# Performance work log

Hardware: AMD Instinct MI355X
Metric: run time of the kernel (lower is better)

## Reference

```python
import jax, jax.numpy as jnp
import numpy as np

N, E = 50000, 800000
F_IN, F_OUT, H, F_EDGE = 256, 32, 8, 5
LEAKY_SLOPE = 0.2


def setup_inputs() -> dict:
    key = jax.random.key(0)
    ks = jax.random.split(key, 6)
    x = jax.random.normal(ks[0], (N, F_IN), dtype=jnp.float32)
    edge_index = jax.random.randint(ks[1], (2, E), 0, N, dtype=jnp.int64)
    edge_attr = jax.random.normal(ks[2], (E, F_EDGE), dtype=jnp.float32)
    degree_src = jax.random.randint(ks[3], (E,), 0, 64, dtype=jnp.int64)
    # Xavier-uniform params
    lim_W = float(np.sqrt(6.0 / (F_IN + F_OUT)))
    W = jax.random.uniform(ks[4], (H, F_IN, F_OUT), minval=-lim_W, maxval=lim_W, dtype=jnp.float32)
    A = 2 * F_OUT + F_EDGE
    lim_a = float(np.sqrt(6.0 / (H + A)))
    a = jax.random.uniform(ks[5], (H, A), minval=-lim_a, maxval=lim_a, dtype=jnp.float32)
    lim_e = float(np.sqrt(1.0 / F_EDGE))
    W_edge_w = jax.random.uniform(jax.random.fold_in(key, 7), (F_EDGE, F_EDGE), minval=-lim_e, maxval=lim_e, dtype=jnp.float32)
    return {"x": x, "edge_index": edge_index, "edge_attr": edge_attr,
            "degree_src": degree_src, "W": W, "a": a, "W_edge_w": W_edge_w}


def reference(x, edge_index, edge_attr, degree_src, W, a, W_edge_w):
    n = x.shape[0]
    h, f_out = W.shape[0], W.shape[2]
    src, dst = edge_index[0], edge_index[1]
    # per-head projection: (N, H, F_out)
    Wh = jnp.einsum('nf,hfo->nho', x, W)
    # split attention vector instead of materializing the concat
    a_src, a_dst, a_e = a[:, :f_out], a[:, f_out:2 * f_out], a[:, 2 * f_out:]
    ef = edge_attr @ W_edge_w.T                      # (E, F_edge)
    e = (jnp.einsum('eho,ho->eh', Wh[src], a_src)
         + jnp.einsum('eho,ho->eh', Wh[dst], a_dst)
         + ef @ a_e.T)                                # (E, H)
    e = jax.nn.leaky_relu(e, LEAKY_SLOPE)
    scale = 1.0 / jnp.sqrt(jnp.clip(degree_src.astype(jnp.float32), 1.0, None))
    e = e * scale[:, None]
    # segment softmax over src; torch scatter_reduce amax include_self=True with zeros init -> max includes 0
    e_max = jnp.maximum(jax.ops.segment_max(e, src, num_segments=n), 0.0)
    e_exp = jnp.exp(e - e_max[src])
    e_sum = jax.ops.segment_sum(e_exp, src, num_segments=n)
    alpha = e_exp / (e_sum[src] + 1e-16)             # (E, H)
    msg = Wh[dst] * alpha[:, :, None]                # (E, H, F_out)
    out = jax.ops.segment_sum(msg, src, num_segments=n)
    out = jax.nn.elu(out.reshape(n, h * f_out))
    return out, alpha
```

## Files before the change

kernel.cpp:

```cpp
#include <hip/hip_runtime.h>
#include <hip/hip_bf16.h>
#include <math.h>

#define NN 50000
#define NE 800000
#define FIN 256
#define FOUT 32
#define NH 8
#define FE 5
#define AROW 69
#define NROWS_PAD 50048
#define NTILES 3128
#define BSTRIDE 48
#define CSTRIDE 264

typedef float f32x4 __attribute__((ext_vector_type(4)));
typedef short bf16x8 __attribute__((ext_vector_type(8)));

static __device__ __forceinline__ unsigned short f2bf(float f) {
    unsigned u = __float_as_uint(f);
    unsigned r = (u + 0x7FFFu + ((u >> 16) & 1u)) >> 16;
    return (unsigned short)r;
}
static __device__ __forceinline__ float bf2f(unsigned short b) {
    return __uint_as_float(((unsigned)b) << 16);
}
static __device__ __forceinline__ short f2bf_fast(float f) {
    __hip_bfloat16 h = __float2bfloat16(f);
    return *reinterpret_cast<short*>(&h);
}

__global__ __launch_bounds__(256) void k_prepre(const float* __restrict__ W,
                                                const float* __restrict__ a,
                                                const float* __restrict__ Wew,
                                                const float* __restrict__ x,
                                                const int* __restrict__ ei,
                                                float* __restrict__ C,
                                                unsigned short* __restrict__ Bhf,
                                                unsigned short* __restrict__ Bsfh,
                                                unsigned short* __restrict__ Bsfl,
                                                unsigned short* __restrict__ xbf,
                                                int* __restrict__ counts,
                                                int* __restrict__ pos) {
    int b = blockIdx.x, t = threadIdx.x;
    int j = b * 256 + t;
    if (j < NROWS_PAD * 32) {
        int row = j >> 5, seg = j & 31;
        bf16x8 hi;
#pragma unroll
        for (int e = 0; e < 8; ++e) hi[e] = 0;
        if (row < NN) {
            const float* sp = &x[(size_t)row * 256 + seg * 8];
            f32x4 u0 = *(const f32x4*)sp;
            f32x4 u1 = *(const f32x4*)(sp + 4);
            hi[0] = f2bf_fast(u0.x); hi[1] = f2bf_fast(u0.y);
            hi[2] = f2bf_fast(u0.z); hi[3] = f2bf_fast(u0.w);
            hi[4] = f2bf_fast(u1.x); hi[5] = f2bf_fast(u1.y);
            hi[6] = f2bf_fast(u1.z); hi[7] = f2bf_fast(u1.w);
        }
        int tile = row >> 4, r = row & 15;
        int ks = seg >> 2, blk = seg & 3;
        *(bf16x8*)&xbf[(size_t)tile * 4096 + ks * 512 + (blk * 16 + r) * 8] = hi;
    }
    if (j < NE / 4) {
        int4 e4 = *(const int4*)&ei[j * 4];
        int4 pv;
        pv.x = atomicAdd(&counts[e4.x], 1);
        pv.y = atomicAdd(&counts[e4.y], 1);
        pv.z = atomicAdd(&counts[e4.z], 1);
        pv.w = atomicAdd(&counts[e4.w], 1);
        *(int4*)&pos[j * 4] = pv;
    }
    if (b < 256) {
        int c = b, k = t;
        int h = c >> 5, o = c & 31;
        unsigned short val = f2bf(W[(size_t)h * (FIN * FOUT) + (size_t)k * FOUT + o]);
        int c_tile = c >> 4, rr = c & 15;
        int ks = k >> 5, bb = (k >> 3) & 3, e = k & 7;
        Bhf[(size_t)c_tile * 4096 + ks * 512 + (bb * 16 + rr) * 8 + e] = val;
    } else if (b == 256) {
        if (t < NH * FE) {
            int h = t / FE, k = t % FE;
            float s = 0.f;
            for (int q = 0; q < FE; ++q) s += a[h * AROW + 2 * FOUT + q] * Wew[q * FE + k];
            C[t] = s;
        }
        int k = t;
        int ks = k >> 5, bb = (k >> 3) & 3, e = k & 7;
        for (int h = 0; h < NH; ++h) {
            float s1v = 0.f, s2v = 0.f;
            for (int o = 0; o < FOUT; ++o) {
                float wv = W[(size_t)h * (FIN * FOUT) + (size_t)k * FOUT + o];
                s1v += wv * a[h * AROW + o];
                s2v += wv * a[h * AROW + FOUT + o];
            }
            unsigned short h1 = f2bf(s1v);
            unsigned short l1 = f2bf(s1v - bf2f(h1));
            unsigned short h2 = f2bf(s2v);
            unsigned short l2v = f2bf(s2v - bf2f(h2));
            Bsfh[ks * 512 + (bb * 16 + h) * 8 + e] = h1;
            Bsfl[ks * 512 + (bb * 16 + h) * 8 + e] = l1;
            Bsfh[ks * 512 + (bb * 16 + 8 + h) * 8 + e] = h2;
            Bsfl[ks * 512 + (bb * 16 + 8 + h) * 8 + e] = l2v;
        }
    }
}

__global__ __launch_bounds__(256) void k_gemm_mfma(const unsigned short* __restrict__ xbf,
                                                   const unsigned short* __restrict__ Bhf,
                                                   const unsigned short* __restrict__ Bsfh,
                                                   const unsigned short* __restrict__ Bsfl,
                                                   unsigned short* __restrict__ Whb,
                                                   float* __restrict__ s1,
                                                   float* __restrict__ s2, int nrows) {
    __shared__ __align__(16) unsigned short Ct[64 * CSTRIDE];
    int t = threadIdx.x;
    int w = t >> 6, l = t & 63;
    int r = l & 15, blk = l >> 4;
    int row0 = blockIdx.x * 64;
    int tile0 = blockIdx.x * 4;
    int c0 = w * 64;

    f32x4 acc[4][4];
    f32x4 acc_s = (f32x4)(0.f);
#pragma unroll
    for (int i = 0; i < 4; ++i)
#pragma unroll
        for (int q = 0; q < 4; ++q) acc[i][q] = (f32x4)(0.f);

    const unsigned short* pa[4];
    const unsigned short* pb[4];
#pragma unroll
    for (int rt = 0; rt < 4; ++rt)
        pa[rt] = xbf + (size_t)(tile0 + rt) * 4096 + l * 8;
#pragma unroll
    for (int ct = 0; ct < 4; ++ct)
        pb[ct] = Bhf + (size_t)(w * 4 + ct) * 4096 + l * 8;
    const unsigned short* psh = Bsfh + l * 8;
    const unsigned short* psl = Bsfl + l * 8;

#pragma unroll
    for (int ks = 0; ks < 8; ++ks) {
        bf16x8 ah[4];
#pragma unroll
        for (int rt = 0; rt < 4; ++rt)
            ah[rt] = *(const bf16x8*)(pa[rt] + ks * 512);
        bf16x8 bh[4];
#pragma unroll
        for (int ct = 0; ct < 4; ++ct)
            bh[ct] = *(const bf16x8*)(pb[ct] + ks * 512);
#pragma unroll
        for (int ct = 0; ct < 4; ++ct) {
#pragma unroll
            for (int rt = 0; rt < 4; ++rt)
                acc[rt][ct] = __builtin_amdgcn_mfma_f32_16x16x32_bf16(ah[rt], bh[ct], acc[rt][ct], 0, 0, 0);
        }
        {
            bf16x8 bsh = *(const bf16x8*)(psh + ks * 512);
            bf16x8 bsl = *(const bf16x8*)(psl + ks * 512);
            acc_s = __builtin_amdgcn_mfma_f32_16x16x32_bf16(ah[w], bsh, acc_s, 0, 0, 0);
            acc_s = __builtin_amdgcn_mfma_f32_16x16x32_bf16(ah[w], bsl, acc_s, 0, 0, 0);
        }
    }

#pragma unroll
    for (int rt = 0; rt < 4; ++rt)
#pragma unroll
        for (int reg = 0; reg < 4; ++reg)
#pragma unroll
            for (int ct = 0; ct < 4; ++ct)
                Ct[(rt * 16 + blk * 4 + reg) * CSTRIDE + c0 + ct * 16 + r] =
                    f2bf(acc[rt][ct][reg]);
    __syncthreads();
#pragma unroll
    for (int i = 0; i < 16; ++i) {
        int row = row0 + w * 16 + i;
        if (row < nrows) {
            ushort4 v = *(const ushort4*)&Ct[(w * 16 + i) * CSTRIDE + l * 4];
            *(ushort4*)&Whb[(size_t)row * 256 + l * 4] = v;
        }
    }
#pragma unroll
    for (int reg = 0; reg < 4; ++reg) {
        int row = row0 + w * 16 + blk * 4 + reg;
        if (row < nrows) {
            if (r < 8) s1[row * NH + r] = acc_s[reg];
            else       s2[row * NH + (r - 8)] = acc_s[reg];
        }
    }
}

__global__ __launch_bounds__(256) void k_scatlog(const int* __restrict__ ei,
                                                 const float* __restrict__ eattr,
                                                 const int* __restrict__ degs,
                                                 const float* __restrict__ s1,
                                                 const float* __restrict__ s2,
                                                 const float* __restrict__ C,
                                                 const int* __restrict__ pos,
                                                 unsigned short* __restrict__ e_perm,
                                                 int2* __restrict__ de_perm) {
    __shared__ float Cl[NH * FE];
    int t = threadIdx.x;
    if (t < NH * FE) Cl[t] = C[t];
    __syncthreads();
    int e = blockIdx.x * 256 + t;
    if (e >= NE) return;
    int src = ei[e], dst = ei[NE + e];
    int dg = degs[e];
    float scale = rsqrtf((float)(dg > 1 ? dg : 1));
    float ea0 = eattr[(size_t)e * FE + 0];
    float ea1 = eattr[(size_t)e * FE + 1];
    float ea2 = eattr[(size_t)e * FE + 2];
    float ea3 = eattr[(size_t)e * FE + 3];
    float ea4 = eattr[(size_t)e * FE + 4];
    float4 s1a = *(const float4*)&s1[src * NH];
    float4 s1b = *(const float4*)&s1[src * NH + 4];
    float4 s2a = *(const float4*)&s2[dst * NH];
    float4 s2b = *(const float4*)&s2[dst * NH + 4];
    float vs1[8] = {s1a.x, s1a.y, s1a.z, s1a.w, s1b.x, s1b.y, s1b.z, s1b.w};
    float vs2[8] = {s2a.x, s2a.y, s2a.z, s2a.w, s2b.x, s2b.y, s2b.z, s2b.w};
    bf16x8 v;
#pragma unroll
    for (int h = 0; h < NH; ++h) {
        float q = vs1[h] + vs2[h] + ea0 * Cl[h * FE + 0] + ea1 * Cl[h * FE + 1] +
                  ea2 * Cl[h * FE + 2] + ea3 * Cl[h * FE + 3] + ea4 * Cl[h * FE + 4];
        q = q > 0.f ? q : 0.2f * q;
        v[h] = (short)f2bf(q * scale);
    }
    int ps = pos[e];
    if (ps < BSTRIDE) {
        int p = src * BSTRIDE + ps;
        *(bf16x8*)&e_perm[(size_t)p * 8] = v;
        de_perm[p] = make_int2(dst, e);
    }
}

__global__ __launch_bounds__(256) void k_smmsg(const int* __restrict__ counts,
                                               const unsigned short* __restrict__ e_perm,
                                               const int2* __restrict__ de_perm,
                                               const unsigned short* __restrict__ Whb,
                                               float* __restrict__ out_alpha,
                                               float* __restrict__ out) {
    __shared__ float al[4][BSTRIDE * 8];
    __shared__ int dl[4][BSTRIDE];
    __shared__ int el[4][BSTRIDE];
    int t = threadIdx.x;
    int w = t >> 6, l = t & 63;
    int n = blockIdx.x * 4 + w;
    if (n >= NN) return;
    int start = n * BSTRIDE;
    int deg = counts[n];
    if (deg > BSTRIDE) deg = BSTRIDE;
    int j = l >> 3, h = l & 7;

    if (l < BSTRIDE) {
        int dv = 0, ev = -1;
        if (l < deg) {
            int2 de = de_perm[start + l];
            dv = de.x; ev = de.y;
        }
        dl[w][l] = dv;
        el[w][l] = ev;
    }
    float vc[6];
#pragma unroll
    for (int q = 0; q < 6; ++q) {
        int b = j + 8 * q;
        vc[q] = (b < deg) ? bf2f(e_perm[(size_t)(start + b) * 8 + h]) : -1e30f;
    }
    float mx = 0.f;
#pragma unroll
    for (int q = 0; q < 6; ++q) mx = fmaxf(mx, vc[q]);
    mx = fmaxf(mx, __shfl_xor(mx, 8));
    mx = fmaxf(mx, __shfl_xor(mx, 16));
    mx = fmaxf(mx, __shfl_xor(mx, 32));
    float m = mx;
    float ex[6];
    float sm = 0.f;
#pragma unroll
    for (int q = 0; q < 6; ++q) { ex[q] = __expf(vc[q] - m); sm += ex[q]; }
    sm += __shfl_xor(sm, 8);
    sm += __shfl_xor(sm, 16);
    sm += __shfl_xor(sm, 32);
    float inv = 1.f / (sm + 1e-16f);
    asm volatile("s_waitcnt lgkmcnt(0)" ::: "memory");
#pragma unroll
    for (int q = 0; q < 6; ++q) {
        int b = j + 8 * q;
        float av = (b < deg) ? ex[q] * inv : 0.f;
        al[w][b * 8 + h] = av;
        if (b < deg) out_alpha[(size_t)el[w][b] * 8 + h] = av;
    }
    asm volatile("s_waitcnt lgkmcnt(0)" ::: "memory");
    f32x4 acc = (f32x4)(0.f);
    int hh = l >> 3;
    int nd8 = (deg + 7) & ~7;
    for (int jj = 0; jj < nd8; jj += 8) {
        int d[8];
        float a8[8];
#pragma unroll
        for (int q = 0; q < 8; ++q) {
            d[q] = dl[w][jj + q];
            a8[q] = al[w][(jj + q) * 8 + hh];
        }
        ushort4 u[8];
#pragma unroll
        for (int q = 0; q < 8; ++q)
            u[q] = *(const ushort4*)&Whb[(size_t)d[q] * 256 + l * 4];
#pragma unroll
        for (int q = 0; q < 8; ++q) {
            acc.x += a8[q] * bf2f(u[q].x);
            acc.y += a8[q] * bf2f(u[q].y);
            acc.z += a8[q] * bf2f(u[q].z);
            acc.w += a8[q] * bf2f(u[q].w);
        }
    }
    f32x4 o;
    o.x = acc.x > 0.f ? acc.x : expm1f(acc.x);
    o.y = acc.y > 0.f ? acc.y : expm1f(acc.y);
    o.z = acc.z > 0.f ? acc.z : expm1f(acc.z);
    o.w = acc.w > 0.f ? acc.w : expm1f(acc.w);
    *(f32x4*)&out[(size_t)n * 256 + l * 4] = o;
}

extern "C" void kernel_launch(void* const* d_in, const int* in_sizes, int n_in,
                              void* d_out, int out_size, void* d_ws, size_t ws_size,
                              hipStream_t stream) {
    const float* x     = (const float*)d_in[0];
    const int*   ei    = (const int*)d_in[1];
    const float* eattr = (const float*)d_in[2];
    const int*   degs  = (const int*)d_in[3];
    const float* W     = (const float*)d_in[4];
    const float* a     = (const float*)d_in[5];
    const float* Wew   = (const float*)d_in[6];

    float* out       = (float*)d_out;
    float* out_alpha = out + (size_t)NN * 256;

    char* p = (char*)d_ws;
    auto alloc = [&](size_t bytes) -> char* {
        char* r = p;
        p += (bytes + 255) & ~(size_t)255;
        return r;
    };
    unsigned short* Whb     = (unsigned short*)alloc((size_t)NN * 256 * 2);
    unsigned short* xbf     = (unsigned short*)alloc((size_t)NTILES * 4096 * 2);
    float*          s1      = (float*)alloc((size_t)NN * NH * 4);
    float*          s2      = (float*)alloc((size_t)NN * NH * 4);
    float*          Cm      = (float*)alloc(NH * FE * 4);
    unsigned short* Bhf     = (unsigned short*)alloc((size_t)16 * 4096 * 2);
    unsigned short* Bsfh    = (unsigned short*)alloc((size_t)4096 * 2);
    unsigned short* Bsfl    = (unsigned short*)alloc((size_t)4096 * 2);
    int*            counts  = (int*)alloc((size_t)NN * 4);
    int*            pos     = (int*)alloc((size_t)NE * 4);
    unsigned short* e_perm  = (unsigned short*)alloc(((size_t)NN * BSTRIDE + 64) * NH * 2);
    int2*           de_perm = (int2*)alloc(((size_t)NN * BSTRIDE + 64) * 8);

    hipMemsetAsync(counts, 0, (size_t)NN * 4, stream);

    k_prepre<<<(NROWS_PAD * 32 + 255) / 256, 256, 0, stream>>>(W, a, Wew, x, ei, Cm, Bhf,
                                                               Bsfh, Bsfl, xbf, counts, pos);
    k_gemm_mfma<<<NROWS_PAD / 64, 256, 0, stream>>>(xbf, Bhf, Bsfh, Bsfl, Whb, s1, s2, NN);
    k_scatlog<<<(NE + 255) / 256, 256, 0, stream>>>(ei, eattr, degs, s1, s2, Cm,
                                                    pos, e_perm, de_perm);
    k_smmsg<<<(NN + 3) / 4, 256, 0, stream>>>(counts, e_perm, de_perm, Whb,
                                              out_alpha, out);
}
```

Before: 234.0 us.

## Fuse edge logit computation into softmax kernel and bucket edges during counting

Removes the separate edge-logit scatter kernel. The counting pass in the prep kernel now writes (dst, edge id) directly into per-source buckets, and the softmax/message kernel computes the logits itself from s1, s2, edge attributes and degree. This drops one kernel launch, the pos array, and the bf16 e_perm round trip through memory. In exchange, logits are kept in fp32 rather than rounded to bf16, and eattr, degs and s2 are now gathered per edge inside the softmax kernel, with extra LDS staging.

After: 263.2 us. 12.5% more time.

```diff
diff --git a/kernel.cpp b/kernel.cpp
--- a/kernel.cpp
+++ b/kernel.cpp
@@ -41,7 +41,7 @@
                                                 unsigned short* __restrict__ Bsfl,
                                                 unsigned short* __restrict__ xbf,
                                                 int* __restrict__ counts,
-                                                int* __restrict__ pos) {
+                                                int2* __restrict__ de_perm) {
     int b = blockIdx.x, t = threadIdx.x;
     int j = b * 256 + t;
     if (j < NROWS_PAD * 32) {
@@ -63,13 +63,18 @@
         *(bf16x8*)&xbf[(size_t)tile * 4096 + ks * 512 + (blk * 16 + r) * 8] = hi;
     }
     if (j < NE / 4) {
-        int4 e4 = *(const int4*)&ei[j * 4];
-        int4 pv;
-        pv.x = atomicAdd(&counts[e4.x], 1);
-        pv.y = atomicAdd(&counts[e4.y], 1);
-        pv.z = atomicAdd(&counts[e4.z], 1);
-        pv.w = atomicAdd(&counts[e4.w], 1);
-        *(int4*)&pos[j * 4] = pv;
+        int4 s4 = *(const int4*)&ei[j * 4];
+        int4 d4 = *(const int4*)&ei[NE + j * 4];
+        int e0 = j * 4;
+        int sl;
+        sl = atomicAdd(&counts[s4.x], 1);
+        if (sl < BSTRIDE) de_perm[s4.x * BSTRIDE + sl] = make_int2(d4.x, e0 + 0);
+        sl = atomicAdd(&counts[s4.y], 1);
+        if (sl < BSTRIDE) de_perm[s4.y * BSTRIDE + sl] = make_int2(d4.y, e0 + 1);
+        sl = atomicAdd(&counts[s4.z], 1);
+        if (sl < BSTRIDE) de_perm[s4.z * BSTRIDE + sl] = make_int2(d4.z, e0 + 2);
+        sl = atomicAdd(&counts[s4.w], 1);
+        if (sl < BSTRIDE) de_perm[s4.w * BSTRIDE + sl] = make_int2(d4.w, e0 + 3);
     }
     if (b < 256) {
         int c = b, k = t;
@@ -190,65 +195,24 @@
     }
 }
 
-__global__ __launch_bounds__(256) void k_scatlog(const int* __restrict__ ei,
-                                                 const float* __restrict__ eattr,
-                                                 const int* __restrict__ degs,
-                                                 const float* __restrict__ s1,
-                                                 const float* __restrict__ s2,
-                                                 const float* __restrict__ C,
-                                                 const int* __restrict__ pos,
-                                                 unsigned short* __restrict__ e_perm,
-                                                 int2* __restrict__ de_perm) {
-    __shared__ float Cl[NH * FE];
-    int t = threadIdx.x;
-    if (t < NH * FE) Cl[t] = C[t];
-    __syncthreads();
-    int e = blockIdx.x * 256 + t;
-    if (e >= NE) return;
-    int src = ei[e], dst = ei[NE + e];
-    int dg = degs[e];
-    float scale = rsqrtf((float)(dg > 1 ? dg : 1));
-    float ea0 = eattr[(size_t)e * FE + 0];
-    float ea1 = eattr[(size_t)e * FE + 1];
-    float ea2 = eattr[(size_t)e * FE + 2];
-    float ea3 = eattr[(size_t)e * FE + 3];
-    float ea4 = eattr[(size_t)e * FE + 4];
-    float4 s1a = *(const float4*)&s1[src * NH];
-    float4 s1b = *(const float4*)&s1[src * NH + 4];
-    float4 s2a = *(const float4*)&s2[dst * NH];
-    float4 s2b = *(const float4*)&s2[dst * NH + 4];
-    float vs1[8] = {s1a.x, s1a.y, s1a.z, s1a.w, s1b.x, s1b.y, s1b.z, s1b.w};
-    float vs2[8] = {s2a.x, s2a.y, s2a.z, s2a.w, s2b.x, s2b.y, s2b.z, s2b.w};
-    bf16x8 v;
-#pragma unroll
-    for (int h = 0; h < NH; ++h) {
-        float q = vs1[h] + vs2[h] + ea0 * Cl[h * FE + 0] + ea1 * Cl[h * FE + 1] +
-                  ea2 * Cl[h * FE + 2] + ea3 * Cl[h * FE + 3] + ea4 * Cl[h * FE + 4];
-        q = q > 0.f ? q : 0.2f * q;
-        v[h] = (short)f2bf(q * scale);
-    }
-    int ps = pos[e];
-    if (ps < BSTRIDE) {
-        int p = src * BSTRIDE + ps;
-        *(bf16x8*)&e_perm[(size_t)p * 8] = v;
-        de_perm[p] = make_int2(dst, e);
-    }
-}
-
 __global__ __launch_bounds__(256) void k_smmsg(const int* __restrict__ counts,
-                                               const unsigned short* __restrict__ e_perm,
                                                const int2* __restrict__ de_perm,
+                                               const float* __restrict__ eattr,
+                                               const int* __restrict__ degs,
+                                               const float* __restrict__ s1,
+                                               const float* __restrict__ s2,
+                                               const float* __restrict__ C,
                                                const unsigned short* __restrict__ Whb,
                                                float* __restrict__ out_alpha,
                                                float* __restrict__ out) {
     __shared__ float al[4][BSTRIDE * 8];
+    __shared__ float eal[4][BSTRIDE * 6];
     __shared__ int dl[4][BSTRIDE];
     __shared__ int el[4][BSTRIDE];
     int t = threadIdx.x;
     int w = t >> 6, l = t & 63;
     int n = blockIdx.x * 4 + w;
     if (n >= NN) return;
-    int start = n * BSTRIDE;
     int deg = counts[n];
     if (deg > BSTRIDE) deg = BSTRIDE;
     int j = l >> 3, h = l & 7;
@@ -256,17 +220,43 @@
     if (l < BSTRIDE) {
         int dv = 0, ev = -1;
         if (l < deg) {
-            int2 de = de_perm[start + l];
+            int2 de = de_perm[n * BSTRIDE + l];
             dv = de.x; ev = de.y;
         }
         dl[w][l] = dv;
         el[w][l] = ev;
     }
+    asm volatile("s_waitcnt lgkmcnt(0)" ::: "memory");
+    if (l < BSTRIDE) {
+        float e0 = 0.f, e1 = 0.f, e2 = 0.f, e3 = 0.f, e4 = 0.f, sc = 0.f;
+        if (l < deg) {
+            int e = el[w][l];
+            const float* ep = &eattr[(size_t)e * FE];
+            e0 = ep[0]; e1 = ep[1]; e2 = ep[2]; e3 = ep[3]; e4 = ep[4];
+            int dg = degs[e];
+            sc = rsqrtf((float)(dg > 1 ? dg : 1));
+        }
+        eal[w][l * 6 + 0] = e0; eal[w][l * 6 + 1] = e1; eal[w][l * 6 + 2] = e2;
+        eal[w][l * 6 + 3] = e3; eal[w][l * 6 + 4] = e4; eal[w][l * 6 + 5] = sc;
+    }
+    float s1h = s1[n * NH + h];
+    float c0 = C[h * FE + 0], c1 = C[h * FE + 1], c2 = C[h * FE + 2];
+    float c3 = C[h * FE + 3], c4 = C[h * FE + 4];
+    asm volatile("s_waitcnt lgkmcnt(0)" ::: "memory");
     float vc[6];
 #pragma unroll
     for (int q = 0; q < 6; ++q) {
         int b = j + 8 * q;
-        vc[q] = (b < deg) ? bf2f(e_perm[(size_t)(start + b) * 8 + h]) : -1e30f;
+        float val = -1e30f;
+        if (b < deg) {
+            float s2v = s2[dl[w][b] * NH + h];
+            float qv = s1h + s2v + eal[w][b * 6 + 0] * c0 + eal[w][b * 6 + 1] * c1 +
+                       eal[w][b * 6 + 2] * c2 + eal[w][b * 6 + 3] * c3 +
+                       eal[w][b * 6 + 4] * c4;
+            qv = qv > 0.f ? qv : 0.2f * qv;
+            val = qv * eal[w][b * 6 + 5];
+        }
+        vc[q] = val;
     }
     float mx = 0.f;
 #pragma unroll
@@ -283,7 +273,6 @@
     sm += __shfl_xor(sm, 16);
     sm += __shfl_xor(sm, 32);
     float inv = 1.f / (sm + 1e-16f);
-    asm volatile("s_waitcnt lgkmcnt(0)" ::: "memory");
 #pragma unroll
     for (int q = 0; q < 6; ++q) {
         int b = j + 8 * q;
@@ -352,17 +341,14 @@
     unsigned short* Bsfh    = (unsigned short*)alloc((size_t)4096 * 2);
     unsigned short* Bsfl    = (unsigned short*)alloc((size_t)4096 * 2);
     int*            counts  = (int*)alloc((size_t)NN * 4);
-    int*            pos     = (int*)alloc((size_t)NE * 4);
-    unsigned short* e_perm  = (unsigned short*)alloc(((size_t)NN * BSTRIDE + 64) * NH * 2);
     int2*           de_perm = (int2*)alloc(((size_t)NN * BSTRIDE + 64) * 8);
 
     hipMemsetAsync(counts, 0, (size_t)NN * 4, stream);
 
     k_prepre<<<(NROWS_PAD * 32 + 255) / 256, 256, 0, stream>>>(W, a, Wew, x, ei, Cm, Bhf,
-                                                               Bsfh, Bsfl, xbf, counts, pos);
+                                                               Bsfh, Bsfl, xbf, counts,
+                                                               de_perm);
     k_gemm_mfma<<<NROWS_PAD / 64, 256, 0, stream>>>(xbf, Bhf, Bsfh, Bsfl, Whb, s1, s2, NN);
-    k_scatlog<<<(NE + 255) / 256, 256, 0, stream>>>(ei, eattr, degs, s1, s2, Cm,
-                                                    pos, e_perm, de_perm);
-    k_smmsg<<<(NN + 3) / 4, 256, 0, stream>>>(counts, e_perm, de_perm, Whb,
-                                              out_alpha, out);
-}
+    k_smmsg<<<(NN + 3) / 4, 256, 0, stream>>>(counts, de_perm, eattr, degs, s1, s2,
+                                              Cm, Whb, out_alpha, out);
+}
```
